# Performance work log

Hardware: AMD Instinct MI355X
Metric: run time of the kernel (lower is better)

The kernel has to match this reference:

```python
import jax, jax.numpy as jnp
import numpy as np

MESSAGE_PASSES = 3
HID = 100        # hidden_node_features == message_size
EDGE_F = 4       # n_edge_features
OUT = 100        # readout output dim


def setup_inputs() -> dict:
    key = jax.random.key(0)
    ks = jax.random.split(key, 8)
    B, N = 32, 128
    nodes = jax.random.normal(ks[0], (B, N, HID), dtype=jnp.float32)
    edges = jax.random.uniform(ks[1], (B, N, N, EDGE_F), dtype=jnp.float32)
    s = 1.0 / np.sqrt(HID)
    Wv = jax.random.normal(ks[2], (HID, HID), dtype=jnp.float32) * s
    Ww = jax.random.normal(ks[3], (HID, HID), dtype=jnp.float32) * s
    We = jax.random.normal(ks[4], (EDGE_F, HID), dtype=jnp.float32) * (1.0 / np.sqrt(EDGE_F))
    Wu = jax.random.normal(ks[5], (2 * HID, HID), dtype=jnp.float32) * (1.0 / np.sqrt(2 * HID))
    Wr = jax.random.normal(ks[6], (2 * HID, OUT), dtype=jnp.float32) * (1.0 / np.sqrt(2 * HID))
    return {"nodes": nodes, "edges": edges, "Wv": Wv, "Ww": Ww, "We": We, "Wu": Wu, "Wr": Wr}


def reference(nodes, edges, Wv, Ww, We, Wu, Wr):
    # adjacency[b,v,w] = sum_e edges[b,v,w,e]; nonzero entries define the edge set
    adjacency = edges.sum(axis=-1)                       # [B,N,N]
    edge_mask = adjacency != 0                           # [B,N,N]
    node_mask = adjacency.sum(axis=-1) != 0              # [B,N]

    # edge feature projection is constant across message passes
    e_proj = jnp.einsum('bvwe,eh->bvwh', edges, We)      # [B,N,N,H]

    hidden = nodes                                       # hidden_node_features == node feat dim
    for _ in range(MESSAGE_PASSES):
        # message_terms for every (b, v, w) edge: relu(h_v Wv + h_w Ww + e_vw We)
        pre = (hidden @ Wv)[:, :, None, :] + (hidden @ Ww)[:, None, :, :] + e_proj
        mterms = jnp.where(edge_mask[..., None], jax.nn.relu(pre), 0.0)
        # (same_batch * same_node) matmul == segment-sum over neighbors w
        messages = mterms.sum(axis=2)                    # [B,N,H]
        # update only nodes that appear in the edge set (degree > 0)
        upd = jnp.tanh(jnp.concatenate([hidden, messages], axis=-1) @ Wu)
        hidden = jnp.where(node_mask[..., None], upd, hidden)

    # readout: masked sum-pool of per-node graph terms
    graph_terms = jax.nn.relu(jnp.concatenate([hidden, nodes], axis=-1) @ Wr)  # [B,N,OUT]
    output = jnp.where(node_mask[..., None], graph_terms, 0.0).sum(axis=1)     # [B,OUT]
    return output
```

## Files before the change

kernel.cpp:

```cpp
#include <hip/hip_runtime.h>
#include <math.h>

#define BATCH 32
#define N 128
#define H 100
#define EF 4

__global__ __launch_bounds__(128) void k_hw(const float* __restrict__ hidden,
                                            const float* __restrict__ Ww,
                                            float* __restrict__ hw) {
    const int row = blockIdx.x;
    const int t = threadIdx.x;
    __shared__ float hid[H];
    if (t < H) hid[t] = hidden[row * H + t];
    __syncthreads();
    if (t < H) {
        float acc = 0.f;
#pragma unroll 4
        for (int k = 0; k < H; ++k) acc = fmaf(hid[k], Ww[k * H + t], acc);
        hw[row * H + t] = acc;
    }
}

__global__ __launch_bounds__(128) void k_msg_upd(const float* __restrict__ edges,
                                                 const float* __restrict__ Wv,
                                                 const float* __restrict__ We,
                                                 const float* __restrict__ Wu,
                                                 const float* __restrict__ hw,
                                                 float* __restrict__ hidden,
                                                 float* __restrict__ node_mask) {
    const int row = blockIdx.x;
    const int b = row >> 7;
    const int t = threadIdx.x;

    __shared__ float hid[H];
    __shared__ float4 erow[N];
    __shared__ float asum[N];
    __shared__ float msg[H];
    __shared__ float nodesum;

    if (t < H) hid[t] = hidden[row * H + t];
    {
        const float4* e4 = (const float4*)(edges + (size_t)row * N * EF);
        float4 e = e4[t];
        erow[t] = e;
        asum[t] = ((e.x + e.y) + e.z) + e.w;
    }
    __syncthreads();

    if (t == 0) {
        float s = 0.f;
        for (int w = 0; w < N; ++w) s += asum[w];
        nodesum = s;
        node_mask[row] = (s != 0.f) ? 1.f : 0.f;
    }

    if (t < H) {
        float hv = 0.f;
#pragma unroll 4
        for (int k = 0; k < H; ++k) hv = fmaf(hid[k], Wv[k * H + t], hv);

        const float we0 = We[t];
        const float we1 = We[H + t];
        const float we2 = We[2 * H + t];
        const float we3 = We[3 * H + t];

        const float* hwb = hw + (size_t)b * N * H + t;
        float acc = 0.f;
#pragma unroll 4
        for (int w = 0; w < N; ++w) {
            const float4 e = erow[w];
            float pre = hv + hwb[w * H];
            pre = fmaf(e.x, we0, pre);
            pre = fmaf(e.y, we1, pre);
            pre = fmaf(e.z, we2, pre);
            pre = fmaf(e.w, we3, pre);
            acc += (asum[w] != 0.f) ? fmaxf(pre, 0.f) : 0.f;
        }
        msg[t] = acc;
    }
    __syncthreads();

    if (t < H) {
        float u = 0.f;
#pragma unroll 4
        for (int k = 0; k < H; ++k) u = fmaf(hid[k], Wu[k * H + t], u);
#pragma unroll 4
        for (int k = 0; k < H; ++k) u = fmaf(msg[k], Wu[(H + k) * H + t], u);
        const float newh = (nodesum != 0.f) ? tanhf(u) : hid[t];
        hidden[row * H + t] = newh;
    }
}

__global__ __launch_bounds__(128) void k_readout(const float* __restrict__ hidden,
                                                 const float* __restrict__ nodes,
                                                 const float* __restrict__ Wr,
                                                 const float* __restrict__ node_mask,
                                                 float* __restrict__ out) {
    const int row = blockIdx.x;
    const int b = row >> 7;
    const int t = threadIdx.x;
    __shared__ float hid[H];
    __shared__ float nod[H];
    if (t < H) {
        hid[t] = hidden[row * H + t];
        nod[t] = nodes[row * H + t];
    }
    __syncthreads();
    if (node_mask[row] == 0.f) return;
    if (t < H) {
        float u = 0.f;
#pragma unroll 4
        for (int k = 0; k < H; ++k) u = fmaf(hid[k], Wr[k * H + t], u);
#pragma unroll 4
        for (int k = 0; k < H; ++k) u = fmaf(nod[k], Wr[(H + k) * H + t], u);
        u = fmaxf(u, 0.f);
        atomicAdd(&out[b * H + t], u);
    }
}

extern "C" void kernel_launch(void* const* d_in, const int* in_sizes, int n_in,
                              void* d_out, int out_size, void* d_ws, size_t ws_size,
                              hipStream_t stream) {
    const float* nodes = (const float*)d_in[0];
    const float* edges = (const float*)d_in[1];
    const float* Wv    = (const float*)d_in[2];
    const float* Ww    = (const float*)d_in[3];
    const float* We    = (const float*)d_in[4];
    const float* Wu    = (const float*)d_in[5];
    const float* Wr    = (const float*)d_in[6];
    float* out = (float*)d_out;

    const int rows = BATCH * N;
    float* hidden = (float*)d_ws;
    float* hwbuf  = hidden + (size_t)rows * H;
    float* nmask  = hwbuf + (size_t)rows * H;

    hipMemcpyAsync(hidden, nodes, (size_t)rows * H * sizeof(float),
                   hipMemcpyDeviceToDevice, stream);
    hipMemsetAsync(d_out, 0, (size_t)out_size * sizeof(float), stream);

    for (int p = 0; p < 3; ++p) {
        k_hw<<<rows, 128, 0, stream>>>(hidden, Ww, hwbuf);
        k_msg_upd<<<rows, 128, 0, stream>>>(edges, Wv, We, Wu, hwbuf, hidden, nmask);
    }
    k_readout<<<rows, 128, 0, stream>>>(hidden, nodes, Wr, nmask, out);
}
```

Baseline: 238.1 us.

## Fuse next-pass Wv/Ww projections into update kernel with ping-pong hw buffers

Restructures the pipeline so each message-pass kernel also computes the next pass's h·Wv and h·Ww projections from the freshly updated hidden state, using ping-pong hw buffers. This removes the separate projection launch per pass and the redundant Wv matvec in the message kernel. Blocks now handle two rows with 256 threads, and the node mask is computed once by a wave-ballot kernel. The initial memcpy is dropped and readout pre-reduces the two rows before its atomic. More work per block may raise register pressure, and the extra __syncthreads adds a serialization point.

```diff
diff --git a/kernel.cpp b/kernel.cpp
--- a/kernel.cpp
+++ b/kernel.cpp
@@ -1,122 +1,175 @@
 #include <hip/hip_runtime.h>
 #include <math.h>
 
-#define BATCH 32
-#define N 128
-#define H 100
-#define EF 4
-
-__global__ __launch_bounds__(128) void k_hw(const float* __restrict__ hidden,
-                                            const float* __restrict__ Ww,
-                                            float* __restrict__ hw) {
-    const int row = blockIdx.x;
-    const int t = threadIdx.x;
-    __shared__ float hid[H];
-    if (t < H) hid[t] = hidden[row * H + t];
-    __syncthreads();
-    if (t < H) {
-        float acc = 0.f;
+#define B_   32
+#define N_   128
+#define H_   100
+#define ROWS (B_ * N_)
+#define RH   (ROWS * H_)
+
+__global__ __launch_bounds__(256) void k_mask(const float* __restrict__ edges,
+                                              float* __restrict__ nmask) {
+    const int t = threadIdx.x, lane = t & 63, wv = t >> 6;
+    const int row = blockIdx.x * 4 + wv;
+    const float4* eg = (const float4*)(edges + (size_t)row * N_ * 4);
+    const float4 e0 = eg[lane], e1 = eg[lane + 64];
+    const float s0 = (e0.x + e0.y) + (e0.z + e0.w);
+    const float s1 = (e1.x + e1.y) + (e1.z + e1.w);
+    const unsigned long long bl = __ballot((s0 != 0.f) || (s1 != 0.f));
+    if (lane == 0) nmask[row] = bl ? 1.f : 0.f;
+}
+
+__global__ __launch_bounds__(256, 6) void k_proj0(const float* __restrict__ nodes,
+                                                  const float* __restrict__ Wv,
+                                                  const float* __restrict__ Ww,
+                                                  float* __restrict__ hv,
+                                                  float* __restrict__ hw) {
+    __shared__ float nod_s[2][H_];
+    const int row0 = blockIdx.x * 2;
+    const int t = threadIdx.x, r = t >> 7, j = t & 127;
+    {
+        const float4* ng = (const float4*)(nodes + (size_t)row0 * H_);
+        if (t < 50) ((float4*)nod_s)[t] = ng[t];
+    }
+    __syncthreads();
+    if (j >= H_) return;
+    const float* hr = nod_s[r];
+    float va = 0.f, wa = 0.f;
 #pragma unroll 4
-        for (int k = 0; k < H; ++k) acc = fmaf(hid[k], Ww[k * H + t], acc);
-        hw[row * H + t] = acc;
-    }
-}
-
-__global__ __launch_bounds__(128) void k_msg_upd(const float* __restrict__ edges,
-                                                 const float* __restrict__ Wv,
+    for (int k = 0; k < H_; ++k) {
+        const float hk = hr[k];
+        va = fmaf(hk, Wv[k * H_ + j], va);
+        wa = fmaf(hk, Ww[k * H_ + j], wa);
+    }
+    hv[(size_t)(row0 + r) * H_ + j] = va;
+    hw[(size_t)(row0 + r) * H_ + j] = wa;
+}
+
+__global__ __launch_bounds__(256, 6) void k_pass(const float* __restrict__ edges,
                                                  const float* __restrict__ We,
                                                  const float* __restrict__ Wu,
-                                                 const float* __restrict__ hw,
+                                                 const float* __restrict__ Wv,
+                                                 const float* __restrict__ Ww,
+                                                 const float* __restrict__ nmask,
+                                                 float* __restrict__ hv_io,
+                                                 const float* __restrict__ hw_in,
+                                                 float* __restrict__ hw_out,
+                                                 const float* __restrict__ hid_in,
                                                  float* __restrict__ hidden,
-                                                 float* __restrict__ node_mask) {
-    const int row = blockIdx.x;
-    const int b = row >> 7;
-    const int t = threadIdx.x;
-
-    __shared__ float hid[H];
-    __shared__ float4 erow[N];
-    __shared__ float asum[N];
-    __shared__ float msg[H];
-    __shared__ float nodesum;
-
-    if (t < H) hid[t] = hidden[row * H + t];
-    {
-        const float4* e4 = (const float4*)(edges + (size_t)row * N * EF);
-        float4 e = e4[t];
-        erow[t] = e;
-        asum[t] = ((e.x + e.y) + e.z) + e.w;
-    }
-    __syncthreads();
-
-    if (t == 0) {
-        float s = 0.f;
-        for (int w = 0; w < N; ++w) s += asum[w];
-        nodesum = s;
-        node_mask[row] = (s != 0.f) ? 1.f : 0.f;
-    }
-
-    if (t < H) {
-        float hv = 0.f;
+                                                 int do_proj) {
+    __shared__ float4 e_s[2][N_];
+    __shared__ float  m_s[2][N_];
+    __shared__ float  hid_s[2][H_];
+    __shared__ float  msg_s[2][H_];
+    __shared__ float  hn_s[2][H_];
+
+    const int row0 = blockIdx.x * 2;
+    const int b = row0 >> 7;
+    const int t = threadIdx.x, r = t >> 7, j = t & 127;
+    const int row = row0 + r;
+
+    {
+        const float4* eg = (const float4*)(edges + (size_t)row0 * N_ * 4);
+        const float4 e = eg[t];
+        e_s[r][j] = e;
+        const float s = (e.x + e.y) + (e.z + e.w);
+        m_s[r][j] = (s != 0.f) ? 1.f : 0.f;
+    }
+    {
+        const float4* hg = (const float4*)(hid_in + (size_t)row0 * H_);
+        if (t < 50) ((float4*)hid_s)[t] = hg[t];
+    }
+    __syncthreads();
+
+    const bool act = (j < H_);
+    if (act) {
+        const float hvv = hv_io[(size_t)row * H_ + j];
+        const float we0 = We[0 * H_ + j], we1 = We[1 * H_ + j];
+        const float we2 = We[2 * H_ + j], we3 = We[3 * H_ + j];
+        const float* hwp = hw_in + (size_t)b * N_ * H_ + j;
+        float acc = 0.f;
+#pragma unroll 8
+        for (int w = 0; w < N_; ++w) {
+            const float  hww = hwp[w * H_];
+            const float4 e = e_s[r][w];
+            const float  m = m_s[r][w];
+            float p = hvv + hww;
+            p = fmaf(e.x, we0, p);
+            p = fmaf(e.y, we1, p);
+            p = fmaf(e.z, we2, p);
+            p = fmaf(e.w, we3, p);
+            acc = fmaf(m, fmaxf(p, 0.f), acc);
+        }
+        msg_s[r][j] = acc;
+    }
+    __syncthreads();
+
+    float nh = 0.f;
+    if (act) {
+        const float* hr = hid_s[r];
+        const float* mr = msg_s[r];
+        float u = 0.f;
+#pragma unroll 8
+        for (int k = 0; k < H_; ++k)
+            u = fmaf(hr[k], Wu[k * H_ + j], u);
+#pragma unroll 8
+        for (int k = 0; k < H_; ++k)
+            u = fmaf(mr[k], Wu[(H_ + k) * H_ + j], u);
+        const float nm = nmask[row];
+        nh = (nm != 0.f) ? tanhf(u) : hr[j];
+        hidden[(size_t)row * H_ + j] = nh;
+        if (do_proj) hn_s[r][j] = nh;
+    }
+
+    if (do_proj) {
+        __syncthreads();
+        if (act) {
+            const float* hr = hn_s[r];
+            float va = 0.f, wa = 0.f;
 #pragma unroll 4
-        for (int k = 0; k < H; ++k) hv = fmaf(hid[k], Wv[k * H + t], hv);
-
-        const float we0 = We[t];
-        const float we1 = We[H + t];
-        const float we2 = We[2 * H + t];
-        const float we3 = We[3 * H + t];
-
-        const float* hwb = hw + (size_t)b * N * H + t;
-        float acc = 0.f;
-#pragma unroll 4
-        for (int w = 0; w < N; ++w) {
-            const float4 e = erow[w];
-            float pre = hv + hwb[w * H];
-            pre = fmaf(e.x, we0, pre);
-            pre = fmaf(e.y, we1, pre);
-            pre = fmaf(e.z, we2, pre);
-            pre = fmaf(e.w, we3, pre);
-            acc += (asum[w] != 0.f) ? fmaxf(pre, 0.f) : 0.f;
+            for (int k = 0; k < H_; ++k) {
+                const float hk = hr[k];
+                va = fmaf(hk, Wv[k * H_ + j], va);
+                wa = fmaf(hk, Ww[k * H_ + j], wa);
+            }
+            hv_io[(size_t)row * H_ + j] = va;
+            hw_out[(size_t)row * H_ + j] = wa;
         }
-        msg[t] = acc;
-    }
-    __syncthreads();
-
-    if (t < H) {
+    }
+}
+
+__global__ __launch_bounds__(256, 6) void k_readout(const float* __restrict__ hidden,
+                                                    const float* __restrict__ nodes,
+                                                    const float* __restrict__ Wr,
+                                                    const float* __restrict__ nmask,
+                                                    float* __restrict__ out) {
+    __shared__ float hid_s[2][H_], nod_s[2][H_], red_s[2][H_];
+    const int row0 = blockIdx.x * 2, b = row0 >> 7;
+    const int t = threadIdx.x, r = t >> 7, j = t & 127;
+    const int row = row0 + r;
+    {
+        const float4* hg = (const float4*)(hidden + (size_t)row0 * H_);
+        const float4* ng = (const float4*)(nodes + (size_t)row0 * H_);
+        if (t < 50) {
+            ((float4*)hid_s)[t] = hg[t];
+            ((float4*)nod_s)[t] = ng[t];
+        }
+    }
+    __syncthreads();
+    if (j < H_) {
+        const float* hr = hid_s[r];
+        const float* nr = nod_s[r];
         float u = 0.f;
-#pragma unroll 4
-        for (int k = 0; k < H; ++k) u = fmaf(hid[k], Wu[k * H + t], u);
-#pragma unroll 4
-        for (int k = 0; k < H; ++k) u = fmaf(msg[k], Wu[(H + k) * H + t], u);
-        const float newh = (nodesum != 0.f) ? tanhf(u) : hid[t];
-        hidden[row * H + t] = newh;
-    }
-}
-
-__global__ __launch_bounds__(128) void k_readout(const float* __restrict__ hidden,
-                                                 const float* __restrict__ nodes,
-                                                 const float* __restrict__ Wr,
-                                                 const float* __restrict__ node_mask,
-                                                 float* __restrict__ out) {
-    const int row = blockIdx.x;
-    const int b = row >> 7;
-    const int t = threadIdx.x;
-    __shared__ float hid[H];
-    __shared__ float nod[H];
-    if (t < H) {
-        hid[t] = hidden[row * H + t];
-        nod[t] = nodes[row * H + t];
-    }
-    __syncthreads();
-    if (node_mask[row] == 0.f) return;
-    if (t < H) {
-        float u = 0.f;
-#pragma unroll 4
-        for (int k = 0; k < H; ++k) u = fmaf(hid[k], Wr[k * H + t], u);
-#pragma unroll 4
-        for (int k = 0; k < H; ++k) u = fmaf(nod[k], Wr[(H + k) * H + t], u);
-        u = fmaxf(u, 0.f);
-        atomicAdd(&out[b * H + t], u);
-    }
+#pragma unroll 8
+        for (int k = 0; k < H_; ++k)
+            u = fmaf(hr[k], Wr[k * H_ + j], u);
+#pragma unroll 8
+        for (int k = 0; k < H_; ++k)
+            u = fmaf(nr[k], Wr[(H_ + k) * H_ + j], u);
+        red_s[r][j] = nmask[row] * fmaxf(u, 0.f);
+    }
+    __syncthreads();
+    if (t < H_) atomicAdd(out + b * H_ + t, red_s[0][t] + red_s[1][t]);
 }
 
 extern "C" void kernel_launch(void* const* d_in, const int* in_sizes, int n_in,
@@ -131,18 +184,23 @@
     const float* Wr    = (const float*)d_in[6];
     float* out = (float*)d_out;
 
-    const int rows = BATCH * N;
     float* hidden = (float*)d_ws;
-    float* hwbuf  = hidden + (size_t)rows * H;
-    float* nmask  = hwbuf + (size_t)rows * H;
-
-    hipMemcpyAsync(hidden, nodes, (size_t)rows * H * sizeof(float),
-                   hipMemcpyDeviceToDevice, stream);
+    float* hv     = hidden + RH;
+    float* hwA    = hv + RH;
+    float* hwB    = hwA + RH;
+    float* nmask  = hwB + RH;
+
     hipMemsetAsync(d_out, 0, (size_t)out_size * sizeof(float), stream);
 
-    for (int p = 0; p < 3; ++p) {
-        k_hw<<<rows, 128, 0, stream>>>(hidden, Ww, hwbuf);
-        k_msg_upd<<<rows, 128, 0, stream>>>(edges, Wv, We, Wu, hwbuf, hidden, nmask);
-    }
-    k_readout<<<rows, 128, 0, stream>>>(hidden, nodes, Wr, nmask, out);
-}
+    k_mask<<<ROWS / 4, 256, 0, stream>>>(edges, nmask);
+    k_proj0<<<ROWS / 2, 256, 0, stream>>>(nodes, Wv, Ww, hv, hwA);
+
+    k_pass<<<ROWS / 2, 256, 0, stream>>>(edges, We, Wu, Wv, Ww, nmask,
+                                         hv, hwA, hwB, nodes, hidden, 1);
+    k_pass<<<ROWS / 2, 256, 0, stream>>>(edges, We, Wu, Wv, Ww, nmask,
+                                         hv, hwB, hwA, hidden, hidden, 1);
+    k_pass<<<ROWS / 2, 256, 0, stream>>>(edges, We, Wu, Wv, Ww, nmask,
+                                         hv, hwA, hwB, hidden, hidden, 0);
+
+    k_readout<<<ROWS / 2, 256, 0, stream>>>(hidden, nodes, Wr, nmask, out);
+}
```

Measured after the change: 212.3 us. 10.9% less time.
